# Kernel optimization log

Hardware: AMD Instinct MI355X
Metric: run time of the kernel (lower is better)

Reference implementation:

```python
import jax, jax.numpy as jnp
import numpy as np

N = 50000      # nodes
E = 800000     # edges
F_IN = 256     # input node features
H = 64         # hidden_dim
C = 10         # num_classes
G = 64         # graphs in batch


def setup_inputs() -> dict:
    key = jax.random.key(0)
    ks = jax.random.split(key, 10)
    x = jax.random.normal(ks[0], (N, F_IN), dtype=jnp.float32)
    edge_index = jax.random.randint(ks[1], (2, E), 0, N, dtype=jnp.int64)
    batch = jnp.sort(jax.random.randint(ks[2], (N,), 0, G, dtype=jnp.int64))
    def glorot(k, fan_in, fan_out):
        return jax.random.normal(k, (fan_in, fan_out), dtype=jnp.float32) / jnp.sqrt(jnp.float32(fan_in))
    return {
        "x": x,
        "edge_index": edge_index,
        "batch": batch,
        "W1": glorot(ks[3], F_IN, H), "b1": jnp.zeros((H,), jnp.float32),
        "W2": glorot(ks[4], H, H),    "b2": jnp.zeros((H,), jnp.float32),
        "W3": glorot(ks[5], H, H),    "b3": jnp.zeros((H,), jnp.float32),
        "lin_W": glorot(ks[6], H, C), "lin_b": jnp.zeros((C,), jnp.float32),
    }


def reference(x, edge_index, batch, W1, b1, W2, b2, W3, b3, lin_W, lin_b):
    src, dst = edge_index[0], edge_index[1]
    # GCN normalization with self-loops: deg counts (A + I) in-degree
    deg = jax.ops.segment_sum(jnp.ones((E,), x.dtype), dst, num_segments=N) + 1.0
    dis = jax.lax.rsqrt(deg)                       # deg^{-1/2}, [N]
    edge_norm = dis[src] * dis[dst]                # [E]
    self_norm = dis * dis                          # [N] (self-loop weight)

    def gcn_conv_relu(h, W, b):
        h = h @ W                                  # [N, H]
        msg = h[src] * edge_norm[:, None]          # gather + scale, [E, H]
        agg = jax.ops.segment_sum(msg, dst, num_segments=N)
        agg = agg + h * self_norm[:, None]         # self-loop contribution
        return jax.nn.relu(agg + b)                # dropout is identity in eval

    h = gcn_conv_relu(x, W1, b1)
    h = gcn_conv_relu(h, W2, b2)
    h = gcn_conv_relu(h, W3, b3)

    # global mean pool over graphs
    counts = jax.ops.segment_sum(jnp.ones((N,), h.dtype), batch, num_segments=G)
    pooled = jax.ops.segment_sum(h, batch, num_segments=G) / jnp.maximum(counts, 1.0)[:, None]
    return pooled @ lin_W + lin_b                  # [G, C]
```

## Files before the change

kernel.cpp:

```cpp
#include <hip/hip_runtime.h>

#define N_NODES 50000
#define N_EDGES 800000
#define F_INPUT 256
#define HDIM 64
#define NCLS 10
#define NGRAPH 64

#define BSHIFT 7
#define NBUCK 391
#define SCAP 4096

typedef float f32x4v __attribute__((ext_vector_type(4)));
typedef short bf16x8 __attribute__((ext_vector_type(8)));

union B8U { uint4 q; bf16x8 v; };

__device__ __forceinline__ float bflo(unsigned v) { return __uint_as_float(v << 16); }
__device__ __forceinline__ float bfhi(unsigned v) { return __uint_as_float(v & 0xFFFF0000u); }
__device__ __forceinline__ unsigned f2b2(float a, float b) {
    unsigned x = __float_as_uint(a); x = (x + 0x7FFF + ((x >> 16) & 1)) >> 16;
    unsigned y = __float_as_uint(b); y = (y + 0x7FFF + ((y >> 16) & 1)) >> 16;
    return x | (y << 16);
}

__device__ __forceinline__ void split2(float x0, float x1, unsigned& h, unsigned& l) {
    unsigned u0 = __float_as_uint(x0), u1 = __float_as_uint(x1);
    unsigned m0 = u0 & 0xFFFF0000u, m1 = u1 & 0xFFFF0000u;
    h = (u0 >> 16) | m1;
    float r0 = x0 - __uint_as_float(m0);
    float r1 = x1 - __uint_as_float(m1);
    l = (__float_as_uint(r0) >> 16) | (__float_as_uint(r1) & 0xFFFF0000u);
}

#define ADD8(b, u)                                    \
    b##0 += bflo(u.x); b##1 += bfhi(u.x);             \
    b##2 += bflo(u.y); b##3 += bfhi(u.y);             \
    b##4 += bflo(u.z); b##5 += bfhi(u.z);             \
    b##6 += bflo(u.w); b##7 += bfhi(u.w);

__global__ __launch_bounds__(256) void k_part(const int* __restrict__ src,
                                              const int* __restrict__ dst,
                                              int* __restrict__ bcnt,
                                              int* __restrict__ stage, int E) {
    __shared__ int cnt[NBUCK];
    __shared__ int base[NBUCK];
    const int tid = threadIdx.x;
    const int e0 = blockIdx.x * 4096;
    int pb[16], pv[16];
    for (int t = tid; t < NBUCK; t += 256) cnt[t] = 0;
    __syncthreads();
#pragma unroll
    for (int j = 0; j < 16; ++j) {
        int e = e0 + j * 256 + tid;
        if (e < E) {
            int s = src[e], d = dst[e];
            pb[j] = d >> BSHIFT;
            pv[j] = (s << BSHIFT) | (d & 127);
            atomicAdd(&cnt[pb[j]], 1);
        } else pb[j] = -1;
    }
    __syncthreads();
    for (int t = tid; t < NBUCK; t += 256) {
        int c = cnt[t];
        base[t] = c ? atomicAdd(&bcnt[t], c) : 0;
        cnt[t] = 0;
    }
    __syncthreads();
#pragma unroll
    for (int j = 0; j < 16; ++j) {
        if (pb[j] >= 0) {
            int r = base[pb[j]] + atomicAdd(&cnt[pb[j]], 1);
            if (r < SCAP) stage[pb[j] * SCAP + r] = pv[j];
        }
    }
}

__global__ __launch_bounds__(256) void k_csr(const int* __restrict__ stage,
                                             const int* __restrict__ bcnt,
                                             float* __restrict__ dis,
                                             int4* __restrict__ rng,
                                             int* __restrict__ eadj, int n) {
    __shared__ int cnt[128];
    __shared__ int loc[128];
    __shared__ int lcur[128];
    __shared__ int ebuf[SCAP];
    const int b = blockIdx.x;
    const int tid = threadIdx.x;
    const int n0 = b << BSHIFT;
    const int nn = min(128, n - n0);
    const int sb = b * SCAP;
    const int len = min(bcnt[b], SCAP);
    if (tid < 128) cnt[tid] = 0;
    __syncthreads();
    for (int j = tid; j < len; j += 256) atomicAdd(&cnt[stage[sb + j] & 127], 1);
    __syncthreads();
    if (tid < 128) loc[tid] = cnt[tid];
    __syncthreads();
    for (int d = 1; d < 128; d <<= 1) {
        int x = 0;
        if (tid < 128 && tid >= d) x = loc[tid - d];
        __syncthreads();
        if (tid < 128) loc[tid] += x;
        __syncthreads();
    }
    if (tid < 128) {
        int ex = loc[tid] - cnt[tid];
        if (tid < nn) {
            int dg = cnt[tid];
            float di = rsqrtf((float)(dg + 1));
            dis[n0 + tid] = di;
            rng[n0 + tid] = make_int4(sb + ex, sb + ex + dg, __float_as_int(di), 0);
        }
        lcur[tid] = ex;
    }
    __syncthreads();
    for (int j = tid; j < len; j += 256) {
        int p = stage[sb + j];
        int rk = atomicAdd(&lcur[p & 127], 1);
        ebuf[rk] = p >> BSHIFT;
    }
    __syncthreads();
    for (int j = tid; j < len; j += 256) eadj[sb + j] = ebuf[j];
}

__global__ __launch_bounds__(256) void k_prepW(const float* __restrict__ W1,
                                               const float* __restrict__ W2,
                                               const float* __restrict__ W3,
                                               uint4* __restrict__ Bf1,
                                               uint4* __restrict__ Bf2,
                                               uint4* __restrict__ Bf3) {
    int s = blockIdx.x * 256 + threadIdx.x;
    const float* W; uint4* out; int local, KS;
    if (s < 2048)      { W = W1; out = Bf1; local = s;        KS = 8; }
    else if (s < 2560) { W = W2; out = Bf2; local = s - 2048; KS = 2; }
    else               { W = W3; out = Bf3; local = s - 2560; KS = 2; }
    const int lane = local & 63;
    const int t    = (local >> 6) & 3;
    const int ks   = local >> 8;
    const int kb   = ks * 32 + ((lane >> 4) << 3);
    const int col  = t * 16 + (lane & 15);
    unsigned h[4], l[4];
#pragma unroll
    for (int j = 0; j < 4; ++j) {
        float x0 = W[(size_t)(kb + 2 * j) * HDIM + col];
        float x1 = W[(size_t)(kb + 2 * j + 1) * HDIM + col];
        split2(x0, x1, h[j], l[j]);
    }
    out[(ks * 4 + t) * 64 + lane]          = make_uint4(h[0], h[1], h[2], h[3]);
    out[((KS + ks) * 4 + t) * 64 + lane]   = make_uint4(l[0], l[1], l[2], l[3]);
}

__global__ __launch_bounds__(256) void k_gemm_mf(const float* __restrict__ A,
                                                 const uint4* __restrict__ Bf,
                                                 const float* __restrict__ dis,
                                                 unsigned short* __restrict__ C,
                                                 int n, int lda, int ktn) {
    const int tid = threadIdx.x;
    const int ln  = tid & 63;
    const int wv  = tid >> 6;
    const int m   = ln & 15;
    const int kg  = ln >> 4;
    const int grow = blockIdx.x * 64 + wv * 16 + m;
    const float* ar = A + (size_t)min(grow, n - 1) * lda + kg * 8;

    f32x4v acc[4];
#pragma unroll
    for (int t = 0; t < 4; ++t)
#pragma unroll
        for (int j = 0; j < 4; ++j) acc[t][j] = 0.0f;

    float4 c0 = *(const float4*)(ar);
    float4 c1 = *(const float4*)(ar + 4);

    for (int ks = 0; ks < ktn; ++ks) {
        const int kn = (ks + 1 < ktn) ? (ks + 1) * 32 : 0;
        float4 p0 = *(const float4*)(ar + kn);
        float4 p1 = *(const float4*)(ar + kn + 4);

        const uint4* bp = Bf + (size_t)ks * 256 + ln;
        const uint4* bq = Bf + (size_t)(ktn + ks) * 256 + ln;
        B8U bh0, bh1, bh2, bh3, bl0, bl1, bl2, bl3;
        bh0.q = bp[0];   bh1.q = bp[64];  bh2.q = bp[128]; bh3.q = bp[192];
        bl0.q = bq[0];   bl1.q = bq[64];  bl2.q = bq[128]; bl3.q = bq[192];

        B8U ah, al;
        split2(c0.x, c0.y, ah.q.x, al.q.x);
        split2(c0.z, c0.w, ah.q.y, al.q.y);
        split2(c1.x, c1.y, ah.q.z, al.q.z);
        split2(c1.z, c1.w, ah.q.w, al.q.w);

        acc[0] = __builtin_amdgcn_mfma_f32_16x16x32_bf16(bh0.v, ah.v, acc[0], 0, 0, 0);
        acc[1] = __builtin_amdgcn_mfma_f32_16x16x32_bf16(bh1.v, ah.v, acc[1], 0, 0, 0);
        acc[2] = __builtin_amdgcn_mfma_f32_16x16x32_bf16(bh2.v, ah.v, acc[2], 0, 0, 0);
        acc[3] = __builtin_amdgcn_mfma_f32_16x16x32_bf16(bh3.v, ah.v, acc[3], 0, 0, 0);
        acc[0] = __builtin_amdgcn_mfma_f32_16x16x32_bf16(bl0.v, ah.v, acc[0], 0, 0, 0);
        acc[1] = __builtin_amdgcn_mfma_f32_16x16x32_bf16(bl1.v, ah.v, acc[1], 0, 0, 0);
        acc[2] = __builtin_amdgcn_mfma_f32_16x16x32_bf16(bl2.v, ah.v, acc[2], 0, 0, 0);
        acc[3] = __builtin_amdgcn_mfma_f32_16x16x32_bf16(bl3.v, ah.v, acc[3], 0, 0, 0);
        acc[0] = __builtin_amdgcn_mfma_f32_16x16x32_bf16(bh0.v, al.v, acc[0], 0, 0, 0);
        acc[1] = __builtin_amdgcn_mfma_f32_16x16x32_bf16(bh1.v, al.v, acc[1], 0, 0, 0);
        acc[2] = __builtin_amdgcn_mfma_f32_16x16x32_bf16(bh2.v, al.v, acc[2], 0, 0, 0);
        acc[3] = __builtin_amdgcn_mfma_f32_16x16x32_bf16(bh3.v, al.v, acc[3], 0, 0, 0);

        c0 = p0; c1 = p1;
    }

    if (grow < n) {
        const float di = dis[grow];
#pragma unroll
        for (int t = 0; t < 4; ++t) {
            uint2 p;
            p.x = f2b2(acc[t][0] * di, acc[t][1] * di);
            p.y = f2b2(acc[t][2] * di, acc[t][3] * di);
            *(uint2*)(C + (size_t)grow * HDIM + t * 16 + kg * 4) = p;
        }
    }
}

__global__ __launch_bounds__(256) void k_gemm_mb(const unsigned short* __restrict__ A,
                                                 const uint4* __restrict__ Bf,
                                                 const float* __restrict__ dis,
                                                 unsigned short* __restrict__ C, int n) {
    const int tid = threadIdx.x;
    const int ln  = tid & 63;
    const int wv  = tid >> 6;
    const int m   = ln & 15;
    const int kg  = ln >> 4;
    const int grow = blockIdx.x * 64 + wv * 16 + m;
    const unsigned short* ar = A + (size_t)min(grow, n - 1) * HDIM + kg * 8;

    f32x4v acc[4];
#pragma unroll
    for (int t = 0; t < 4; ++t)
#pragma unroll
        for (int j = 0; j < 4; ++j) acc[t][j] = 0.0f;

#pragma unroll
    for (int ks = 0; ks < 2; ++ks) {
        B8U af;
        af.q = *(const uint4*)(ar + ks * 32);
        const uint4* bp = Bf + ks * 256 + ln;
        const uint4* bq = Bf + (2 + ks) * 256 + ln;
        B8U bh0, bh1, bh2, bh3, bl0, bl1, bl2, bl3;
        bh0.q = bp[0];  bh1.q = bp[64];  bh2.q = bp[128]; bh3.q = bp[192];
        bl0.q = bq[0];  bl1.q = bq[64];  bl2.q = bq[128]; bl3.q = bq[192];

        acc[0] = __builtin_amdgcn_mfma_f32_16x16x32_bf16(bh0.v, af.v, acc[0], 0, 0, 0);
        acc[1] = __builtin_amdgcn_mfma_f32_16x16x32_bf16(bh1.v, af.v, acc[1], 0, 0, 0);
        acc[2] = __builtin_amdgcn_mfma_f32_16x16x32_bf16(bh2.v, af.v, acc[2], 0, 0, 0);
        acc[3] = __builtin_amdgcn_mfma_f32_16x16x32_bf16(bh3.v, af.v, acc[3], 0, 0, 0);
        acc[0] = __builtin_amdgcn_mfma_f32_16x16x32_bf16(bl0.v, af.v, acc[0], 0, 0, 0);
        acc[1] = __builtin_amdgcn_mfma_f32_16x16x32_bf16(bl1.v, af.v, acc[1], 0, 0, 0);
        acc[2] = __builtin_amdgcn_mfma_f32_16x16x32_bf16(bl2.v, af.v, acc[2], 0, 0, 0);
        acc[3] = __builtin_amdgcn_mfma_f32_16x16x32_bf16(bl3.v, af.v, acc[3], 0, 0, 0);
    }

    if (grow < n) {
        const float di = dis[grow];
#pragma unroll
        for (int t = 0; t < 4; ++t) {
            uint2 p;
            p.x = f2b2(acc[t][0] * di, acc[t][1] * di);
            p.y = f2b2(acc[t][2] * di, acc[t][3] * di);
            *(uint2*)(C + (size_t)grow * HDIM + t * 16 + kg * 4) = p;
        }
    }
}

__global__ __launch_bounds__(256) void k_gather_b(const unsigned short* __restrict__ h,
                                                  const int* __restrict__ eadj,
                                                  const int4* __restrict__ rng,
                                                  const float* __restrict__ bias,
                                                  unsigned short* __restrict__ out, int n) {
    int t = blockIdx.x * 256 + threadIdx.x;
    int i = t >> 3;
    if (i >= n) return;
    const int q = (t & 7) * 8;
    const int4 r = rng[i];
    int e = r.x; const int e1 = r.y;
    const float di = __int_as_float(r.z);
    float a0 = 0.f, a1 = 0.f, a2 = 0.f, a3 = 0.f, a4 = 0.f, a5 = 0.f, a6 = 0.f, a7 = 0.f;
    float g0 = 0.f, g1 = 0.f, g2 = 0.f, g3 = 0.f, g4 = 0.f, g5 = 0.f, g6 = 0.f, g7 = 0.f;
#pragma unroll 2
    for (; e + 3 < e1; e += 4) {
        int s0 = eadj[e];
        int s1 = eadj[e + 1];
        int s2 = eadj[e + 2];
        int s3 = eadj[e + 3];
        uint4 u0 = *(const uint4*)(h + (size_t)s0 * HDIM + q);
        uint4 u1 = *(const uint4*)(h + (size_t)s1 * HDIM + q);
        uint4 u2 = *(const uint4*)(h + (size_t)s2 * HDIM + q);
        uint4 u3 = *(const uint4*)(h + (size_t)s3 * HDIM + q);
        ADD8(a, u0)
        ADD8(g, u1)
        ADD8(a, u2)
        ADD8(g, u3)
    }
    for (; e < e1; ++e) {
        int s0 = eadj[e];
        uint4 u0 = *(const uint4*)(h + (size_t)s0 * HDIM + q);
        ADD8(a, u0)
    }
    uint4 us = *(const uint4*)(h + (size_t)i * HDIM + q);
    ADD8(a, us)
    a0 += g0; a1 += g1; a2 += g2; a3 += g3;
    a4 += g4; a5 += g5; a6 += g6; a7 += g7;
    float4 bl = *(const float4*)(bias + q);
    float4 bh = *(const float4*)(bias + q + 4);
    a0 = fmaxf(fmaf(a0, di, bl.x), 0.f);
    a1 = fmaxf(fmaf(a1, di, bl.y), 0.f);
    a2 = fmaxf(fmaf(a2, di, bl.z), 0.f);
    a3 = fmaxf(fmaf(a3, di, bl.w), 0.f);
    a4 = fmaxf(fmaf(a4, di, bh.x), 0.f);
    a5 = fmaxf(fmaf(a5, di, bh.y), 0.f);
    a6 = fmaxf(fmaf(a6, di, bh.z), 0.f);
    a7 = fmaxf(fmaf(a7, di, bh.w), 0.f);
    uint4 o;
    o.x = f2b2(a0, a1); o.y = f2b2(a2, a3);
    o.z = f2b2(a4, a5); o.w = f2b2(a6, a7);
    *(uint4*)(out + (size_t)i * HDIM + q) = o;
}

__global__ __launch_bounds__(256) void k_gather_pool(const unsigned short* __restrict__ h,
                                                     const int* __restrict__ eadj,
                                                     const int4* __restrict__ rng,
                                                     const float* __restrict__ bias,
                                                     const int* __restrict__ batch,
                                                     float* __restrict__ pooled, int n) {
    __shared__ float sp[NGRAPH][HDIM];
    const int tid = threadIdx.x;
    int t = blockIdx.x * 256 + tid;
    int i = t >> 3;
    const bool valid = (i < n);
    int q = (t & 7) * 8;
    const int i0 = (blockIdx.x * 256) >> 3;
    const int i1 = min(i0 + 32, n);
    const int gmin = batch[min(i0, n - 1)];
    const int gmax = batch[i1 - 1];
    for (int j = tid; j < NGRAPH * HDIM; j += 256) ((float*)sp)[j] = 0.f;
    __syncthreads();
    if (valid) {
        const int4 r = rng[i];
        int e = r.x; const int e1 = r.y;
        const float di = __int_as_float(r.z);
        float a0 = 0.f, a1 = 0.f, a2 = 0.f, a3 = 0.f, a4 = 0.f, a5 = 0.f, a6 = 0.f, a7 = 0.f;
        float g0 = 0.f, g1 = 0.f, g2 = 0.f, g3 = 0.f, g4 = 0.f, g5 = 0.f, g6 = 0.f, g7 = 0.f;
#pragma unroll 2
        for (; e + 3 < e1; e += 4) {
            int s0 = eadj[e];
            int s1 = eadj[e + 1];
            int s2 = eadj[e + 2];
            int s3 = eadj[e + 3];
            uint4 u0 = *(const uint4*)(h + (size_t)s0 * HDIM + q);
            uint4 u1 = *(const uint4*)(h + (size_t)s1 * HDIM + q);
            uint4 u2 = *(const uint4*)(h + (size_t)s2 * HDIM + q);
            uint4 u3 = *(const uint4*)(h + (size_t)s3 * HDIM + q);
            ADD8(a, u0)
            ADD8(g, u1)
            ADD8(a, u2)
            ADD8(g, u3)
        }
        for (; e < e1; ++e) {
            int s0 = eadj[e];
            uint4 u0 = *(const uint4*)(h + (size_t)s0 * HDIM + q);
            ADD8(a, u0)
        }
        uint4 us = *(const uint4*)(h + (size_t)i * HDIM + q);
        ADD8(a, us)
        a0 += g0; a1 += g1; a2 += g2; a3 += g3;
        a4 += g4; a5 += g5; a6 += g6; a7 += g7;
        float4 bl = *(const float4*)(bias + q);
        float4 bh = *(const float4*)(bias + q + 4);
        a0 = fmaxf(fmaf(a0, di, bl.x), 0.f);
        a1 = fmaxf(fmaf(a1, di, bl.y), 0.f);
        a2 = fmaxf(fmaf(a2, di, bl.z), 0.f);
        a3 = fmaxf(fmaf(a3, di, bl.w), 0.f);
        a4 = fmaxf(fmaf(a4, di, bh.x), 0.f);
        a5 = fmaxf(fmaf(a5, di, bh.y), 0.f);
        a6 = fmaxf(fmaf(a6, di, bh.z), 0.f);
        a7 = fmaxf(fmaf(a7, di, bh.w), 0.f);
        int g = batch[i];
        atomicAdd(&sp[g][q + 0], a0); atomicAdd(&sp[g][q + 1], a1);
        atomicAdd(&sp[g][q + 2], a2); atomicAdd(&sp[g][q + 3], a3);
        atomicAdd(&sp[g][q + 4], a4); atomicAdd(&sp[g][q + 5], a5);
        atomicAdd(&sp[g][q + 6], a6); atomicAdd(&sp[g][q + 7], a7);
    }
    __syncthreads();
    int rows = gmax - gmin + 1;
    for (int j = tid; j < rows * HDIM; j += 256) {
        int r = j >> 6, c = j & 63;
        float v = sp[gmin + r][c];
        if (v != 0.f) atomicAdd(&pooled[(gmin + r) * HDIM + c], v);
    }
}

__global__ __launch_bounds__(640) void k_head(const float* __restrict__ pooled,
                                              const int* __restrict__ batch,
                                              const float* __restrict__ linW,
                                              const float* __restrict__ linb,
                                              float* __restrict__ out, int n) {
    int t = threadIdx.x;
    if (t >= NGRAPH * NCLS) return;
    int g = t / NCLS;
    int c = t - g * NCLS;
    int lo = 0, hi = n;
    while (lo < hi) { int m = (lo + hi) >> 1; if (batch[m] < g) lo = m + 1; else hi = m; }
    int s = lo;
    lo = 0; hi = n;
    while (lo < hi) { int m = (lo + hi) >> 1; if (batch[m] < g + 1) lo = m + 1; else hi = m; }
    float inv = 1.0f / fmaxf((float)(lo - s), 1.0f);
    float acc = linb[c];
#pragma unroll
    for (int k = 0; k < HDIM; ++k)
        acc = fmaf(pooled[g * HDIM + k] * inv, linW[k * NCLS + c], acc);
    out[g * NCLS + c] = acc;
}

extern "C" void kernel_launch(void* const* d_in, const int* in_sizes, int n_in,
                              void* d_out, int out_size, void* d_ws, size_t ws_size,
                              hipStream_t stream) {
    (void)in_sizes; (void)n_in; (void)out_size; (void)ws_size;
    const float* x    = (const float*)d_in[0];
    const int*   ei   = (const int*)d_in[1];
    const int*   batch= (const int*)d_in[2];
    const float* W1   = (const float*)d_in[3];
    const float* b1   = (const float*)d_in[4];
    const float* W2   = (const float*)d_in[5];
    const float* b2   = (const float*)d_in[6];
    const float* W3   = (const float*)d_in[7];
    const float* b3   = (const float*)d_in[8];
    const float* linW = (const float*)d_in[9];
    const float* linb = (const float*)d_in[10];
    float* out = (float*)d_out;

    const int N = N_NODES, E = N_EDGES;
    const int* src = ei;
    const int* dst = ei + E;

    char* ws = (char*)d_ws;
    unsigned short* hA = (unsigned short*)ws; ws += (size_t)N * HDIM * 2;
    unsigned short* hB = (unsigned short*)ws; ws += (size_t)N * HDIM * 2;
    float* dis    = (float*)ws; ws += (size_t)N * 4;
    int*   eadj   = (int*)ws;   ws += (size_t)NBUCK * SCAP * 4;
    int*   stage  = (int*)ws;   ws += (size_t)NBUCK * SCAP * 4;
    int4*  rng    = (int4*)ws;  ws += (size_t)N * 16;
    int*   bcnt   = (int*)ws;   ws += ((size_t)NBUCK * 4 + 15) & ~(size_t)15;
    float* pooled = (float*)ws; ws += (size_t)NGRAPH * HDIM * 4;
    uint4* Bf1    = (uint4*)ws; ws += (size_t)2 * 8 * 4 * 64 * 16;
    uint4* Bf2    = (uint4*)ws; ws += (size_t)2 * 2 * 4 * 64 * 16;
    uint4* Bf3    = (uint4*)ws; ws += (size_t)2 * 2 * 4 * 64 * 16;

    const int nbE = (E + 4095) / 4096;
    const int gb  = (N + 63) / 64;
    const int ngth = (N * 8 + 255) / 256;

    hipMemsetAsync(bcnt, 0, (size_t)NBUCK * 4, stream);
    hipMemsetAsync(pooled, 0, (size_t)NGRAPH * HDIM * 4, stream);
    k_prepW<<<12, 256, 0, stream>>>(W1, W2, W3, Bf1, Bf2, Bf3);
    k_part<<<nbE, 256, 0, stream>>>(src, dst, bcnt, stage, E);
    k_csr<<<NBUCK, 256, 0, stream>>>(stage, bcnt, dis, rng, eadj, N);

    k_gemm_mf<<<gb, 256, 0, stream>>>(x, Bf1, dis, hA, N, F_INPUT, 8);
    k_gather_b<<<ngth, 256, 0, stream>>>(hA, eadj, rng, b1, hB, N);
    k_gemm_mb<<<gb, 256, 0, stream>>>(hB, Bf2, dis, hA, N);
    k_gather_b<<<ngth, 256, 0, stream>>>(hA, eadj, rng, b2, hB, N);
    k_gemm_mb<<<gb, 256, 0, stream>>>(hB, Bf3, dis, hA, N);
    k_gather_pool<<<ngth, 256, 0, stream>>>(hA, eadj, rng, b3, batch, pooled, N);
    k_head<<<1, 640, 0, stream>>>(pooled, batch, linW, linb, out, N);
}
```

Before: 248.2 us.

## Sort nodes by degree for load-balanced gather in GCN layers

New measurement: 255.5 us. 1.03x slower.

```diff
diff --git a/kernel.cpp b/kernel.cpp
--- a/kernel.cpp
+++ b/kernel.cpp
@@ -10,6 +10,7 @@
 #define BSHIFT 7
 #define NBUCK 391
 #define SCAP 4096
+#define DPB 196
 
 typedef float f32x4v __attribute__((ext_vector_type(4)));
 typedef short bf16x8 __attribute__((ext_vector_type(8)));
@@ -80,10 +81,12 @@
                                              const int* __restrict__ bcnt,
                                              float* __restrict__ dis,
                                              int4* __restrict__ rng,
-                                             int* __restrict__ eadj, int n) {
+                                             int* __restrict__ eadj,
+                                             int* __restrict__ dhist, int n) {
     __shared__ int cnt[128];
     __shared__ int loc[128];
     __shared__ int lcur[128];
+    __shared__ int dh[64];
     __shared__ int ebuf[SCAP];
     const int b = blockIdx.x;
     const int tid = threadIdx.x;
@@ -92,6 +95,7 @@
     const int sb = b * SCAP;
     const int len = min(bcnt[b], SCAP);
     if (tid < 128) cnt[tid] = 0;
+    if (tid < 64) dh[tid] = 0;
     __syncthreads();
     for (int j = tid; j < len; j += 256) atomicAdd(&cnt[stage[sb + j] & 127], 1);
     __syncthreads();
@@ -111,10 +115,12 @@
             float di = rsqrtf((float)(dg + 1));
             dis[n0 + tid] = di;
             rng[n0 + tid] = make_int4(sb + ex, sb + ex + dg, __float_as_int(di), 0);
+            atomicAdd(&dh[min(dg, 63)], 1);
         }
         lcur[tid] = ex;
     }
     __syncthreads();
+    if (tid < 64 && dh[tid]) atomicAdd(&dhist[tid], dh[tid]);
     for (int j = tid; j < len; j += 256) {
         int p = stage[sb + j];
         int rk = atomicAdd(&lcur[p & 127], 1);
@@ -151,11 +157,43 @@
     out[((KS + ks) * 4 + t) * 64 + lane]   = make_uint4(l[0], l[1], l[2], l[3]);
 }
 
-__global__ __launch_bounds__(256) void k_gemm_mf(const float* __restrict__ A,
-                                                 const uint4* __restrict__ Bf,
-                                                 const float* __restrict__ dis,
-                                                 unsigned short* __restrict__ C,
-                                                 int n, int lda, int ktn) {
+__global__ __launch_bounds__(256) void k_gemm_mfp(const float* __restrict__ A,
+                                                  const uint4* __restrict__ Bf,
+                                                  const float* __restrict__ dis,
+                                                  unsigned short* __restrict__ C,
+                                                  int n, int lda, int ktn,
+                                                  const int4* __restrict__ rng,
+                                                  const int* __restrict__ dhist,
+                                                  int* __restrict__ dcur,
+                                                  int* __restrict__ perm, int gbN) {
+    if ((int)blockIdx.x >= gbN) {
+        __shared__ int lh[64], lbase[64], sc[64], dval[64];
+        const int tid = threadIdx.x;
+        const int bb = blockIdx.x - gbN;
+        if (tid < 64) lh[tid] = 0;
+        __syncthreads();
+        int i = bb * 256 + tid;
+        int bin = 0, rk = 0;
+        if (i < n) {
+            int4 r = rng[i];
+            bin = min(r.y - r.x, 63);
+            rk = atomicAdd(&lh[bin], 1);
+        }
+        __syncthreads();
+        if (tid < 64) { int v = dhist[tid]; dval[tid] = v; sc[tid] = v; }
+        __syncthreads();
+        for (int d = 1; d < 64; d <<= 1) {
+            int x = 0;
+            if (tid < 64 && tid >= d) x = sc[tid - d];
+            __syncthreads();
+            if (tid < 64) sc[tid] += x;
+            __syncthreads();
+        }
+        if (tid < 64) lbase[tid] = lh[tid] ? atomicAdd(&dcur[tid], lh[tid]) : 0;
+        __syncthreads();
+        if (i < n) perm[(sc[bin] - dval[bin]) + lbase[bin] + rk] = i;
+        return;
+    }
     const int tid = threadIdx.x;
     const int ln  = tid & 63;
     const int wv  = tid >> 6;
@@ -271,11 +309,13 @@
 __global__ __launch_bounds__(256) void k_gather_b(const unsigned short* __restrict__ h,
                                                   const int* __restrict__ eadj,
                                                   const int4* __restrict__ rng,
+                                                  const int* __restrict__ perm,
                                                   const float* __restrict__ bias,
                                                   unsigned short* __restrict__ out, int n) {
     int t = blockIdx.x * 256 + threadIdx.x;
-    int i = t >> 3;
-    if (i >= n) return;
+    int ii = t >> 3;
+    if (ii >= n) return;
+    const int i = perm[ii];
     const int q = (t & 7) * 8;
     const int4 r = rng[i];
     int e = r.x; const int e1 = r.y;
@@ -445,26 +485,30 @@
     int*   eadj   = (int*)ws;   ws += (size_t)NBUCK * SCAP * 4;
     int*   stage  = (int*)ws;   ws += (size_t)NBUCK * SCAP * 4;
     int4*  rng    = (int4*)ws;  ws += (size_t)N * 16;
-    int*   bcnt   = (int*)ws;   ws += ((size_t)NBUCK * 4 + 15) & ~(size_t)15;
+    int*   perm   = (int*)ws;   ws += (size_t)N * 4;
+    int*   bcnt   = (int*)ws;   ws += ((size_t)(NBUCK + 128) * 4 + 15) & ~(size_t)15;
     float* pooled = (float*)ws; ws += (size_t)NGRAPH * HDIM * 4;
     uint4* Bf1    = (uint4*)ws; ws += (size_t)2 * 8 * 4 * 64 * 16;
     uint4* Bf2    = (uint4*)ws; ws += (size_t)2 * 2 * 4 * 64 * 16;
     uint4* Bf3    = (uint4*)ws; ws += (size_t)2 * 2 * 4 * 64 * 16;
+    int* dhist = bcnt + NBUCK;
+    int* dcur  = bcnt + NBUCK + 64;
 
     const int nbE = (E + 4095) / 4096;
     const int gb  = (N + 63) / 64;
     const int ngth = (N * 8 + 255) / 256;
 
-    hipMemsetAsync(bcnt, 0, (size_t)NBUCK * 4, stream);
+    hipMemsetAsync(bcnt, 0, (size_t)(NBUCK + 128) * 4, stream);
     hipMemsetAsync(pooled, 0, (size_t)NGRAPH * HDIM * 4, stream);
     k_prepW<<<12, 256, 0, stream>>>(W1, W2, W3, Bf1, Bf2, Bf3);
     k_part<<<nbE, 256, 0, stream>>>(src, dst, bcnt, stage, E);
-    k_csr<<<NBUCK, 256, 0, stream>>>(stage, bcnt, dis, rng, eadj, N);
-
-    k_gemm_mf<<<gb, 256, 0, stream>>>(x, Bf1, dis, hA, N, F_INPUT, 8);
-    k_gather_b<<<ngth, 256, 0, stream>>>(hA, eadj, rng, b1, hB, N);
+    k_csr<<<NBUCK, 256, 0, stream>>>(stage, bcnt, dis, rng, eadj, dhist, N);
+
+    k_gemm_mfp<<<gb + DPB, 256, 0, stream>>>(x, Bf1, dis, hA, N, F_INPUT, 8,
+                                             rng, dhist, dcur, perm, gb);
+    k_gather_b<<<ngth, 256, 0, stream>>>(hA, eadj, rng, perm, b1, hB, N);
     k_gemm_mb<<<gb, 256, 0, stream>>>(hB, Bf2, dis, hA, N);
-    k_gather_b<<<ngth, 256, 0, stream>>>(hA, eadj, rng, b2, hB, N);
+    k_gather_b<<<ngth, 256, 0, stream>>>(hA, eadj, rng, perm, b2, hB, N);
     k_gemm_mb<<<gb, 256, 0, stream>>>(hB, Bf3, dis, hA, N);
     k_gather_pool<<<ngth, 256, 0, stream>>>(hA, eadj, rng, b3, batch, pooled, N);
     k_head<<<1, 640, 0, stream>>>(pooled, batch, linW, linb, out, N);
```

## Fuse neighbor gather with next-layer GEMM via LDS and fold memsets into prep kernel

Applied to the files above, without the earlier changes.

Result: faster. 226.9 us (-8.6%).

```diff
diff --git a/kernel.cpp b/kernel.cpp
--- a/kernel.cpp
+++ b/kernel.cpp
@@ -124,13 +124,17 @@
     for (int j = tid; j < len; j += 256) eadj[sb + j] = ebuf[j];
 }
 
-__global__ __launch_bounds__(256) void k_prepW(const float* __restrict__ W1,
+__global__ __launch_bounds__(256) void k_prepZ(const float* __restrict__ W1,
                                                const float* __restrict__ W2,
                                                const float* __restrict__ W3,
                                                uint4* __restrict__ Bf1,
                                                uint4* __restrict__ Bf2,
-                                               uint4* __restrict__ Bf3) {
+                                               uint4* __restrict__ Bf3,
+                                               int* __restrict__ bcnt,
+                                               float* __restrict__ pooled) {
     int s = blockIdx.x * 256 + threadIdx.x;
+    for (int j = s; j < NBUCK; j += 3072) bcnt[j] = 0;
+    for (int j = s; j < NGRAPH * HDIM; j += 3072) pooled[j] = 0.f;
     const float* W; uint4* out; int local, KS;
     if (s < 2048)      { W = W1; out = Bf1; local = s;        KS = 8; }
     else if (s < 2560) { W = W2; out = Bf2; local = s - 2048; KS = 2; }
@@ -218,108 +222,101 @@
     }
 }
 
-__global__ __launch_bounds__(256) void k_gemm_mb(const unsigned short* __restrict__ A,
-                                                 const uint4* __restrict__ Bf,
-                                                 const float* __restrict__ dis,
-                                                 unsigned short* __restrict__ C, int n) {
+__global__ __launch_bounds__(256) void k_fgg(const unsigned short* __restrict__ h,
+                                             const int* __restrict__ eadj,
+                                             const int4* __restrict__ rng,
+                                             const float* __restrict__ bias,
+                                             const uint4* __restrict__ Bf,
+                                             const float* __restrict__ dis,
+                                             unsigned short* __restrict__ out, int n) {
+    __shared__ uint4 rl[32 * 8];
     const int tid = threadIdx.x;
-    const int ln  = tid & 63;
-    const int wv  = tid >> 6;
-    const int m   = ln & 15;
-    const int kg  = ln >> 4;
-    const int grow = blockIdx.x * 64 + wv * 16 + m;
-    const unsigned short* ar = A + (size_t)min(grow, n - 1) * HDIM + kg * 8;
-
-    f32x4v acc[4];
-#pragma unroll
-    for (int t = 0; t < 4; ++t)
-#pragma unroll
-        for (int j = 0; j < 4; ++j) acc[t][j] = 0.0f;
-
+    const int i0 = blockIdx.x * 32;
+    const int node = tid >> 3;
+    const int l8 = tid & 7;
+    const int i = i0 + node;
+    uint4 o = make_uint4(0u, 0u, 0u, 0u);
+    if (i < n) {
+        const int q = l8 * 8;
+        const int4 r = rng[i];
+        int e = r.x; const int e1 = r.y;
+        const float di = __int_as_float(r.z);
+        float a0 = 0.f, a1 = 0.f, a2 = 0.f, a3 = 0.f, a4 = 0.f, a5 = 0.f, a6 = 0.f, a7 = 0.f;
+        float g0 = 0.f, g1 = 0.f, g2 = 0.f, g3 = 0.f, g4 = 0.f, g5 = 0.f, g6 = 0.f, g7 = 0.f;
+#pragma unroll 2
+        for (; e + 3 < e1; e += 4) {
+            int s0 = eadj[e];
+            int s1 = eadj[e + 1];
+            int s2 = eadj[e + 2];
+            int s3 = eadj[e + 3];
+            uint4 u0 = *(const uint4*)(h + (size_t)s0 * HDIM + q);
+            uint4 u1 = *(const uint4*)(h + (size_t)s1 * HDIM + q);
+            uint4 u2 = *(const uint4*)(h + (size_t)s2 * HDIM + q);
+            uint4 u3 = *(const uint4*)(h + (size_t)s3 * HDIM + q);
+            ADD8(a, u0)
+            ADD8(g, u1)
+            ADD8(a, u2)
+            ADD8(g, u3)
+        }
+        for (; e < e1; ++e) {
+            int s0 = eadj[e];
+            uint4 u0 = *(const uint4*)(h + (size_t)s0 * HDIM + q);
+            ADD8(a, u0)
+        }
+        uint4 us = *(const uint4*)(h + (size_t)i * HDIM + q);
+        ADD8(a, us)
+        a0 += g0; a1 += g1; a2 += g2; a3 += g3;
+        a4 += g4; a5 += g5; a6 += g6; a7 += g7;
+        float4 bl = *(const float4*)(bias + q);
+        float4 bh = *(const float4*)(bias + q + 4);
+        a0 = fmaxf(fmaf(a0, di, bl.x), 0.f);
+        a1 = fmaxf(fmaf(a1, di, bl.y), 0.f);
+        a2 = fmaxf(fmaf(a2, di, bl.z), 0.f);
+        a3 = fmaxf(fmaf(a3, di, bl.w), 0.f);
+        a4 = fmaxf(fmaf(a4, di, bh.x), 0.f);
+        a5 = fmaxf(fmaf(a5, di, bh.y), 0.f);
+        a6 = fmaxf(fmaf(a6, di, bh.z), 0.f);
+        a7 = fmaxf(fmaf(a7, di, bh.w), 0.f);
+        o.x = f2b2(a0, a1); o.y = f2b2(a2, a3);
+        o.z = f2b2(a4, a5); o.w = f2b2(a6, a7);
+    }
+    rl[node * 8 + (l8 ^ (node & 7))] = o;
+    __syncthreads();
+
+    const int ln = tid & 63;
+    const int wv = tid >> 6;
+    const int m  = ln & 15;
+    const int kg = ln >> 4;
+    const int row = (wv >> 1) * 16 + m;
+    const int ct0 = (wv & 1) * 2;
+    f32x4v acc0, acc1;
+#pragma unroll
+    for (int j = 0; j < 4; ++j) { acc0[j] = 0.f; acc1[j] = 0.f; }
 #pragma unroll
     for (int ks = 0; ks < 2; ++ks) {
         B8U af;
-        af.q = *(const uint4*)(ar + ks * 32);
+        af.q = rl[row * 8 + ((ks * 4 + kg) ^ (row & 7))];
         const uint4* bp = Bf + ks * 256 + ln;
         const uint4* bq = Bf + (2 + ks) * 256 + ln;
-        B8U bh0, bh1, bh2, bh3, bl0, bl1, bl2, bl3;
-        bh0.q = bp[0];  bh1.q = bp[64];  bh2.q = bp[128]; bh3.q = bp[192];
-        bl0.q = bq[0];  bl1.q = bq[64];  bl2.q = bq[128]; bl3.q = bq[192];
-
-        acc[0] = __builtin_amdgcn_mfma_f32_16x16x32_bf16(bh0.v, af.v, acc[0], 0, 0, 0);
-        acc[1] = __builtin_amdgcn_mfma_f32_16x16x32_bf16(bh1.v, af.v, acc[1], 0, 0, 0);
-        acc[2] = __builtin_amdgcn_mfma_f32_16x16x32_bf16(bh2.v, af.v, acc[2], 0, 0, 0);
-        acc[3] = __builtin_amdgcn_mfma_f32_16x16x32_bf16(bh3.v, af.v, acc[3], 0, 0, 0);
-        acc[0] = __builtin_amdgcn_mfma_f32_16x16x32_bf16(bl0.v, af.v, acc[0], 0, 0, 0);
-        acc[1] = __builtin_amdgcn_mfma_f32_16x16x32_bf16(bl1.v, af.v, acc[1], 0, 0, 0);
-        acc[2] = __builtin_amdgcn_mfma_f32_16x16x32_bf16(bl2.v, af.v, acc[2], 0, 0, 0);
-        acc[3] = __builtin_amdgcn_mfma_f32_16x16x32_bf16(bl3.v, af.v, acc[3], 0, 0, 0);
-    }
-
+        B8U bh0, bh1, bl0, bl1;
+        bh0.q = bp[ct0 * 64]; bh1.q = bp[(ct0 + 1) * 64];
+        bl0.q = bq[ct0 * 64]; bl1.q = bq[(ct0 + 1) * 64];
+        acc0 = __builtin_amdgcn_mfma_f32_16x16x32_bf16(bh0.v, af.v, acc0, 0, 0, 0);
+        acc1 = __builtin_amdgcn_mfma_f32_16x16x32_bf16(bh1.v, af.v, acc1, 0, 0, 0);
+        acc0 = __builtin_amdgcn_mfma_f32_16x16x32_bf16(bl0.v, af.v, acc0, 0, 0, 0);
+        acc1 = __builtin_amdgcn_mfma_f32_16x16x32_bf16(bl1.v, af.v, acc1, 0, 0, 0);
+    }
+    const int grow = i0 + row;
     if (grow < n) {
         const float di = dis[grow];
-#pragma unroll
-        for (int t = 0; t < 4; ++t) {
-            uint2 p;
-            p.x = f2b2(acc[t][0] * di, acc[t][1] * di);
-            p.y = f2b2(acc[t][2] * di, acc[t][3] * di);
-            *(uint2*)(C + (size_t)grow * HDIM + t * 16 + kg * 4) = p;
-        }
-    }
-}
-
-__global__ __launch_bounds__(256) void k_gather_b(const unsigned short* __restrict__ h,
-                                                  const int* __restrict__ eadj,
-                                                  const int4* __restrict__ rng,
-                                                  const float* __restrict__ bias,
-                                                  unsigned short* __restrict__ out, int n) {
-    int t = blockIdx.x * 256 + threadIdx.x;
-    int i = t >> 3;
-    if (i >= n) return;
-    const int q = (t & 7) * 8;
-    const int4 r = rng[i];
-    int e = r.x; const int e1 = r.y;
-    const float di = __int_as_float(r.z);
-    float a0 = 0.f, a1 = 0.f, a2 = 0.f, a3 = 0.f, a4 = 0.f, a5 = 0.f, a6 = 0.f, a7 = 0.f;
-    float g0 = 0.f, g1 = 0.f, g2 = 0.f, g3 = 0.f, g4 = 0.f, g5 = 0.f, g6 = 0.f, g7 = 0.f;
-#pragma unroll 2
-    for (; e + 3 < e1; e += 4) {
-        int s0 = eadj[e];
-        int s1 = eadj[e + 1];
-        int s2 = eadj[e + 2];
-        int s3 = eadj[e + 3];
-        uint4 u0 = *(const uint4*)(h + (size_t)s0 * HDIM + q);
-        uint4 u1 = *(const uint4*)(h + (size_t)s1 * HDIM + q);
-        uint4 u2 = *(const uint4*)(h + (size_t)s2 * HDIM + q);
-        uint4 u3 = *(const uint4*)(h + (size_t)s3 * HDIM + q);
-        ADD8(a, u0)
-        ADD8(g, u1)
-        ADD8(a, u2)
-        ADD8(g, u3)
-    }
-    for (; e < e1; ++e) {
-        int s0 = eadj[e];
-        uint4 u0 = *(const uint4*)(h + (size_t)s0 * HDIM + q);
-        ADD8(a, u0)
-    }
-    uint4 us = *(const uint4*)(h + (size_t)i * HDIM + q);
-    ADD8(a, us)
-    a0 += g0; a1 += g1; a2 += g2; a3 += g3;
-    a4 += g4; a5 += g5; a6 += g6; a7 += g7;
-    float4 bl = *(const float4*)(bias + q);
-    float4 bh = *(const float4*)(bias + q + 4);
-    a0 = fmaxf(fmaf(a0, di, bl.x), 0.f);
-    a1 = fmaxf(fmaf(a1, di, bl.y), 0.f);
-    a2 = fmaxf(fmaf(a2, di, bl.z), 0.f);
-    a3 = fmaxf(fmaf(a3, di, bl.w), 0.f);
-    a4 = fmaxf(fmaf(a4, di, bh.x), 0.f);
-    a5 = fmaxf(fmaf(a5, di, bh.y), 0.f);
-    a6 = fmaxf(fmaf(a6, di, bh.z), 0.f);
-    a7 = fmaxf(fmaf(a7, di, bh.w), 0.f);
-    uint4 o;
-    o.x = f2b2(a0, a1); o.y = f2b2(a2, a3);
-    o.z = f2b2(a4, a5); o.w = f2b2(a6, a7);
-    *(uint4*)(out + (size_t)i * HDIM + q) = o;
+        uint2 p;
+        p.x = f2b2(acc0[0] * di, acc0[1] * di);
+        p.y = f2b2(acc0[2] * di, acc0[3] * di);
+        *(uint2*)(out + (size_t)grow * HDIM + ct0 * 16 + kg * 4) = p;
+        p.x = f2b2(acc1[0] * di, acc1[1] * di);
+        p.y = f2b2(acc1[2] * di, acc1[3] * di);
+        *(uint2*)(out + (size_t)grow * HDIM + (ct0 + 1) * 16 + kg * 4) = p;
+    }
 }
 
 __global__ __launch_bounds__(256) void k_gather_pool(const unsigned short* __restrict__ h,
@@ -453,19 +450,15 @@
 
     const int nbE = (E + 4095) / 4096;
     const int gb  = (N + 63) / 64;
-    const int ngth = (N * 8 + 255) / 256;
-
-    hipMemsetAsync(bcnt, 0, (size_t)NBUCK * 4, stream);
-    hipMemsetAsync(pooled, 0, (size_t)NGRAPH * HDIM * 4, stream);
-    k_prepW<<<12, 256, 0, stream>>>(W1, W2, W3, Bf1, Bf2, Bf3);
+    const int nF  = (N + 31) / 32;
+
+    k_prepZ<<<12, 256, 0, stream>>>(W1, W2, W3, Bf1, Bf2, Bf3, bcnt, pooled);
     k_part<<<nbE, 256, 0, stream>>>(src, dst, bcnt, stage, E);
     k_csr<<<NBUCK, 256, 0, stream>>>(stage, bcnt, dis, rng, eadj, N);
 
     k_gemm_mf<<<gb, 256, 0, stream>>>(x, Bf1, dis, hA, N, F_INPUT, 8);
-    k_gather_b<<<ngth, 256, 0, stream>>>(hA, eadj, rng, b1, hB, N);
-    k_gemm_mb<<<gb, 256, 0, stream>>>(hB, Bf2, dis, hA, N);
-    k_gather_b<<<ngth, 256, 0, stream>>>(hA, eadj, rng, b2, hB, N);
-    k_gemm_mb<<<gb, 256, 0, stream>>>(hB, Bf3, dis, hA, N);
-    k_gather_pool<<<ngth, 256, 0, stream>>>(hA, eadj, rng, b3, batch, pooled, N);
+    k_fgg<<<nF, 256, 0, stream>>>(hA, eadj, rng, b1, Bf2, dis, hB, N);
+    k_fgg<<<nF, 256, 0, stream>>>(hB, eadj, rng, b2, Bf3, dis, hA, N);
+    k_gather_pool<<<nF, 256, 0, stream>>>(hA, eadj, rng, b3, batch, pooled, N);
     k_head<<<1, 640, 0, stream>>>(pooled, batch, linW, linb, out, N);
 }
```
